# Kernel optimization log

Hardware: AMD Instinct MI355X
Metric: run time of the kernel (lower is better)

Reference implementation:

```python
import jax, jax.numpy as jnp
import numpy as np

N = 100000  # nodes


def setup_inputs() -> dict:
    key = jax.random.key(0)
    k0, k1, k2, k3 = jax.random.split(key, 4)
    IN, H, OUT = 256, 256, 128  # in_channels, 2*out_channels, out_channels
    E = 1600000
    x = jax.random.normal(k0, (N, IN), dtype=jnp.float32)
    edge_index = jax.random.randint(k1, (2, E), 0, N, dtype=jnp.int32)
    W1 = jax.random.normal(k2, (IN, H), dtype=jnp.float32) / np.sqrt(IN)
    b1 = jnp.zeros((H,), dtype=jnp.float32)
    W2 = jax.random.normal(k3, (H, OUT), dtype=jnp.float32) / np.sqrt(H)
    b2 = jnp.zeros((OUT,), dtype=jnp.float32)
    return {"x": x, "edge_index": edge_index, "W1": W1, "b1": b1, "W2": W2, "b2": b2}


def _gcn_layer(x, W, b, src, dst, norm):
    # PyG GCNConv: out[i] = sum_{(j->i)} norm_e * (x @ W)[j] + b, over A + I
    h = x @ W
    msg = h[src] * norm[:, None]          # [E+N, F] gathered edge messages
    out = jax.ops.segment_sum(msg, dst, num_segments=N)
    return out + b


def reference(x, edge_index, W1, b1, W2, b2):
    src, dst = edge_index[0], edge_index[1]
    loop = jnp.arange(N, dtype=src.dtype)
    src = jnp.concatenate([src, loop])    # add self-loops
    dst = jnp.concatenate([dst, loop])
    # symmetric normalization: deg computed on target (col) with unit weights
    deg = jax.ops.segment_sum(jnp.ones_like(dst, dtype=x.dtype), dst, num_segments=N)
    dinv = jnp.where(deg > 0, jax.lax.rsqrt(deg), 0.0)
    norm = dinv[src] * dinv[dst]
    h = jax.nn.relu(_gcn_layer(x, W1, b1, src, dst, norm))
    out = jax.nn.relu(_gcn_layer(h, W2, b2, src, dst, norm))
    return out
```

## Files before the change

kernel.cpp:

```cpp
#include <hip/hip_runtime.h>
#include <hip/hip_fp16.h>


typedef _Float16 f16x8 __attribute__((ext_vector_type(8)));
typedef float f32x4 __attribute__((ext_vector_type(4)));
typedef int i32x4 __attribute__((ext_vector_type(4)));
typedef float fv4 __attribute__((ext_vector_type(4)));

constexpr int CAP = 48;
constexpr int FILL_CHUNK = 2048;


__device__ inline void pack_w_body(const float* __restrict__ W, __half* __restrict__ Wp,
                                   int NC, int t) {
    const int NT = NC / 16;
    int lane = t & 63;
    int rest = t >> 6;
    int nt = rest % NT;
    int ks = rest / NT;
    int n = nt * 16 + (lane & 15);
    int k0 = ks * 32 + (lane >> 4) * 8;
    __half tmp[8];
#pragma unroll
    for (int j = 0; j < 8; ++j) tmp[j] = __float2half_rn(W[(size_t)(k0 + j) * NC + n]);
    ((uint4*)Wp)[t] = *(const uint4*)tmp;
}

__global__ __launch_bounds__(256) void prep_kernel(const int* __restrict__ src,
                                                   const int* __restrict__ dst, int E,
                                                   int* __restrict__ cntP, int chP,
                                                   int* __restrict__ colFixed,
                                                   const float* __restrict__ x,
                                                   __half* __restrict__ xh, int n8,
                                                   const float* __restrict__ W1,
                                                   __half* __restrict__ Wp1,
                                                   const float* __restrict__ W2,
                                                   __half* __restrict__ Wp2,
                                                   int nbFill, int nbPack) {
    const int b = blockIdx.x;
    const int tid = threadIdx.x;
    if (b < nbFill) {
        const int sel = b & 7;
        const int chunk = b >> 3;
        const int e0 = chunk * FILL_CHUNK + tid * 8;
        int* __restrict__ myCnt = cntP + sel * chP;
        if (e0 + 8 <= E) {
            i32x4 da = __builtin_nontemporal_load((const i32x4*)(dst + e0));
            i32x4 db = __builtin_nontemporal_load((const i32x4*)(dst + e0) + 1);
            i32x4 sa = __builtin_nontemporal_load((const i32x4*)(src + e0));
            i32x4 sb = __builtin_nontemporal_load((const i32x4*)(src + e0) + 1);
            int d[8] = {da[0], da[1], da[2], da[3], db[0], db[1], db[2], db[3]};
            int s[8] = {sa[0], sa[1], sa[2], sa[3], sb[0], sb[1], sb[2], sb[3]};
#pragma unroll
            for (int j = 0; j < 8; ++j) {
                if ((d[j] & 7) == sel) {
                    int slot = atomicAdd(&myCnt[d[j] >> 3], 1);
                    if (slot < CAP) colFixed[(size_t)d[j] * CAP + slot] = s[j];
                }
            }
        } else {
            for (int j = 0; j < 8; ++j) {
                int e = e0 + j;
                if (e < E) {
                    int dd = dst[e];
                    if ((dd & 7) == sel) {
                        int slot = atomicAdd(&myCnt[dd >> 3], 1);
                        if (slot < CAP) colFixed[(size_t)dd * CAP + slot] = src[e];
                    }
                }
            }
        }
    } else if (b < nbFill + nbPack) {
        int i = (b - nbFill) * 256 + tid;
        if (i < n8) {
            fv4 a = __builtin_nontemporal_load((const fv4*)x + (size_t)i * 2);
            fv4 bb = __builtin_nontemporal_load((const fv4*)x + (size_t)i * 2 + 1);
            __half2 h[4];
            h[0] = __floats2half2_rn(a[0], a[1]);
            h[1] = __floats2half2_rn(a[2], a[3]);
            h[2] = __floats2half2_rn(bb[0], bb[1]);
            h[3] = __floats2half2_rn(bb[2], bb[3]);
            ((uint4*)xh)[i] = *(const uint4*)h;
        }
    } else if (b < nbFill + nbPack + 32) {
        int t = (b - nbFill - nbPack) * 256 + tid;
        pack_w_body(W1, Wp1, 256, t);
    } else {
        int t = (b - nbFill - nbPack - 32) * 256 + tid;
        pack_w_body(W2, Wp2, 128, t);
    }
}

__global__ __launch_bounds__(256) void finish_deg(const int* __restrict__ cntP, int chP,
                                                  float* __restrict__ dinv,
                                                  int* __restrict__ degc, int N) {
    int i = blockIdx.x * 256 + threadIdx.x;
    if (i < N) {
        int c = cntP[(i & 7) * chP + (i >> 3)];
        dinv[i] = rsqrtf((float)(c + 1));
        degc[i] = (c < CAP) ? c : CAP;
    }
}

__global__ __launch_bounds__(256) void aggregate256_h(const __half* __restrict__ xh,
                                                      const float* __restrict__ dinv,
                                                      const int* __restrict__ degc,
                                                      const int* __restrict__ colFixed,
                                                      __half* __restrict__ out, int N) {
    const int lane = threadIdx.x & 63;
    const int i = blockIdx.x * 4 + (threadIdx.x >> 6);
    if (i >= N) return;
    const float di = dinv[i];
    const int deg = degc[i];
    const uint2* __restrict__ hv = (const uint2*)xh;
    uint2 raw = hv[(size_t)i * 64 + lane];
    float2 f0 = __half22float2(*(const __half2*)&raw.x);
    float2 f1 = __half22float2(*(const __half2*)&raw.y);
    float ax = di * f0.x, ay = di * f0.y, az = di * f1.x, aw = di * f1.y;
    const int* __restrict__ cl = colFixed + (size_t)i * CAP;
    int e = 0;
    for (; e + 8 <= deg; e += 8) {
        int s[8];
#pragma unroll
        for (int j = 0; j < 8; ++j) s[j] = cl[e + j];
        float w[8];
#pragma unroll
        for (int j = 0; j < 8; ++j) w[j] = dinv[s[j]];
        uint2 u[8];
#pragma unroll
        for (int j = 0; j < 8; ++j) u[j] = hv[(size_t)s[j] * 64 + lane];
#pragma unroll
        for (int j = 0; j < 8; ++j) {
            float2 g0 = __half22float2(*(const __half2*)&u[j].x);
            float2 g1 = __half22float2(*(const __half2*)&u[j].y);
            ax = fmaf(w[j], g0.x, ax);
            ay = fmaf(w[j], g0.y, ay);
            az = fmaf(w[j], g1.x, az);
            aw = fmaf(w[j], g1.y, aw);
        }
    }
    for (; e < deg; ++e) {
        int s = cl[e];
        float w = dinv[s];
        uint2 u = hv[(size_t)s * 64 + lane];
        float2 g0 = __half22float2(*(const __half2*)&u.x);
        float2 g1 = __half22float2(*(const __half2*)&u.y);
        ax = fmaf(w, g0.x, ax);
        ay = fmaf(w, g0.y, ay);
        az = fmaf(w, g1.x, az);
        aw = fmaf(w, g1.y, aw);
    }
    __half2 h0 = __floats2half2_rn(ax * di, ay * di);
    __half2 h1 = __floats2half2_rn(az * di, aw * di);
    uint2 o;
    o.x = *(const unsigned int*)&h0;
    o.y = *(const unsigned int*)&h1;
    ((uint2*)out)[(size_t)i * 64 + lane] = o;
}

__global__ __launch_bounds__(256) void gemm12_lds(const __half* __restrict__ A,
                                                  const __half* __restrict__ Wp1,
                                                  const float* __restrict__ bias1,
                                                  const __half* __restrict__ Wp2,
                                                  const float* __restrict__ dinv,
                                                  __half* __restrict__ out, int M) {
    constexpr int PITCH = 264;
    __shared__ _Float16 hs[4][16][PITCH];

    const int lane = threadIdx.x & 63;
    const int wave = threadIdx.x >> 6;
    const int kg = lane >> 4;
    const int r = lane & 15;
    const int row = blockIdx.x * 64 + wave * 16 + r;
    const int rowc = (row < M) ? row : (M - 1);

    f32x4 acc1[16];
#pragma unroll
    for (int nt = 0; nt < 16; ++nt) acc1[nt] = {0.f, 0.f, 0.f, 0.f};

    const f16x8* __restrict__ Ap = (const f16x8*)(A + (size_t)rowc * 256 + kg * 8);
    const f16x8* __restrict__ Wf1 = (const f16x8*)Wp1;
#pragma unroll
    for (int ks = 0; ks < 8; ++ks) {
        f16x8 xfrag = Ap[ks * 4];
        const f16x8* wrow = Wf1 + (size_t)(ks * 16) * 64 + lane;
#pragma unroll
        for (int nt = 0; nt < 16; ++nt) {
            f16x8 wfrag = wrow[nt * 64];
            acc1[nt] = __builtin_amdgcn_mfma_f32_16x16x32_f16(wfrag, xfrag, acc1[nt], 0, 0, 0);
        }
    }

#pragma unroll
    for (int nt = 0; nt < 16; ++nt) {
        float4 bb = *(const float4*)(bias1 + nt * 16 + kg * 4);
        f32x4 v = acc1[nt];
        v[0] = fmaxf(v[0] + bb.x, 0.f);
        v[1] = fmaxf(v[1] + bb.y, 0.f);
        v[2] = fmaxf(v[2] + bb.z, 0.f);
        v[3] = fmaxf(v[3] + bb.w, 0.f);
        __half2 h0 = __floats2half2_rn(v[0], v[1]);
        __half2 h1 = __floats2half2_rn(v[2], v[3]);
        uint2 o;
        o.x = *(const unsigned int*)&h0;
        o.y = *(const unsigned int*)&h1;
        *(uint2*)&hs[wave][r][nt * 16 + kg * 4] = o;
    }

    f32x4 acc2[8];
#pragma unroll
    for (int nt = 0; nt < 8; ++nt) acc2[nt] = {0.f, 0.f, 0.f, 0.f};

    const f16x8* __restrict__ Wf2 = (const f16x8*)Wp2;
#pragma unroll
    for (int ks = 0; ks < 8; ++ks) {
        f16x8 xfrag = *(const f16x8*)&hs[wave][r][ks * 32 + kg * 8];
        const f16x8* wrow = Wf2 + (size_t)(ks * 8) * 64 + lane;
#pragma unroll
        for (int nt = 0; nt < 8; ++nt) {
            f16x8 wfrag = wrow[nt * 64];
            acc2[nt] = __builtin_amdgcn_mfma_f32_16x16x32_f16(wfrag, xfrag, acc2[nt], 0, 0, 0);
        }
    }

    if (row < M) {
        float rs = dinv[row];
#pragma unroll
        for (int nt = 0; nt < 8; ++nt) {
            const int n0 = nt * 16 + kg * 4;
            f32x4 v = acc2[nt];
            __half2 h0 = __floats2half2_rn(v[0] * rs, v[1] * rs);
            __half2 h1 = __floats2half2_rn(v[2] * rs, v[3] * rs);
            uint2 o;
            o.x = *(const unsigned int*)&h0;
            o.y = *(const unsigned int*)&h1;
            *(uint2*)(out + (size_t)row * 128 + n0) = o;
        }
    }
}

__global__ __launch_bounds__(256) void aggregate128_h_bias_relu(const __half* __restrict__ h,
                                                                const float* __restrict__ dinv,
                                                                const int* __restrict__ degc,
                                                                const int* __restrict__ colFixed,
                                                                const float* __restrict__ bias,
                                                                float* __restrict__ out, int N) {
    const int lane = threadIdx.x & 63;
    const int i = blockIdx.x * 4 + (threadIdx.x >> 6);
    if (i >= N) return;
    const float di = dinv[i];
    const int deg = degc[i];
    const unsigned int* __restrict__ hv = (const unsigned int*)h;
    float2 v = __half22float2(*(const __half2*)&hv[(size_t)i * 64 + lane]);
    float ax = v.x, ay = v.y;
    const int* __restrict__ cl = colFixed + (size_t)i * CAP;
    int e = 0;
    for (; e + 8 <= deg; e += 8) {
        int s[8];
#pragma unroll
        for (int j = 0; j < 8; ++j) s[j] = cl[e + j];
        unsigned int u[8];
#pragma unroll
        for (int j = 0; j < 8; ++j) u[j] = hv[(size_t)s[j] * 64 + lane];
#pragma unroll
        for (int j = 0; j < 8; ++j) {
            float2 g = __half22float2(*(const __half2*)&u[j]);
            ax += g.x;
            ay += g.y;
        }
    }
    for (; e < deg; ++e) {
        float2 g = __half22float2(*(const __half2*)&hv[(size_t)cl[e] * 64 + lane]);
        ax += g.x;
        ay += g.y;
    }
    float2 bb = ((const float2*)bias)[lane];
    float2 r;
    r.x = fmaxf(fmaf(ax, di, bb.x), 0.f);
    r.y = fmaxf(fmaf(ay, di, bb.y), 0.f);
    ((float2*)out)[(size_t)i * 64 + lane] = r;
}

extern "C" void kernel_launch(void* const* d_in, const int* in_sizes, int n_in,
                              void* d_out, int out_size, void* d_ws, size_t ws_size,
                              hipStream_t stream) {
    const float* x  = (const float*)d_in[0];
    const int*   ei = (const int*)d_in[1];
    const float* W1 = (const float*)d_in[2];
    const float* b1 = (const float*)d_in[3];
    const float* W2 = (const float*)d_in[4];
    const float* b2 = (const float*)d_in[5];
    float* out = (float*)d_out;

    const int N = in_sizes[0] / 256;
    const int E = in_sizes[1] / 2;
    const int* src = ei;
    const int* dst = ei + E;

    char* ws = (char*)d_ws;
    size_t off = 0;
    auto alloc = [&](size_t bytes) -> char* {
        char* p = ws + off;
        off += (bytes + 255) & ~(size_t)255;
        return p;
    };
    const int chP = (N + 7) / 8;
    int*    cntP     = (int*)alloc((size_t)chP * 8 * 4);
    float*  dinv     = (float*)alloc((size_t)N * 4);
    int*    degc     = (int*)alloc((size_t)N * 4);
    int*    colFixed = (int*)alloc((size_t)N * CAP * 4);
    __half* Wp1      = (__half*)alloc((size_t)256 * 256 * 2);
    __half* Wp2      = (__half*)alloc((size_t)256 * 128 * 2);
    __half* bufA     = (__half*)alloc((size_t)N * 256 * 2);
    __half* bufB     = (__half*)alloc((size_t)N * 256 * 2);
    __half* xh    = bufA;
    __half* buf2h = bufA;
    __half* buf1h = bufB;

    hipMemsetAsync(cntP, 0, (size_t)chP * 8 * 4, stream);

    const int n8 = (N * 256) / 8;
    const int nbFill = 8 * ((E + FILL_CHUNK - 1) / FILL_CHUNK);
    const int nbPack = (n8 + 255) / 256;
    const int nbPrep = nbFill + nbPack + 32 + 16;
    prep_kernel<<<nbPrep, 256, 0, stream>>>(src, dst, E, cntP, chP, colFixed, x, xh, n8,
                                            W1, Wp1, W2, Wp2, nbFill, nbPack);

    finish_deg<<<(N + 255) / 256, 256, 0, stream>>>(cntP, chP, dinv, degc, N);

    const int AB = (N + 3) / 4;
    const int GB = (N + 63) / 64;

    aggregate256_h<<<AB, 256, 0, stream>>>(xh, dinv, degc, colFixed, buf1h, N);
    gemm12_lds<<<GB, 256, 0, stream>>>(buf1h, Wp1, b1, Wp2, dinv, buf2h, N);
    aggregate128_h_bias_relu<<<AB, 256, 0, stream>>>(buf2h, dinv, degc, colFixed, b2, out, N);
}
```

Measured before the change: 419.8 us.

## Slice feature matrix into 16-column panels for cache-local first-layer aggregation

Stores the fp16 input features in a sliced layout of 16 panels, each holding 16 columns for every node. The first aggregation kernel now launches one block set per panel, so each gather touches a 3.2 MB panel that can stay in L2/MALL instead of whole 512-byte rows. Within a wave, eight groups of lanes split the edge list and combine their sums with a shuffle reduction. The GEMM reads its A operand from the sliced layout. In exchange the kernel launches 16x more blocks, re-reads the column lists and dinv once per panel, and leaves lanes idle for low-degree nodes.

```diff
diff --git a/kernel.cpp b/kernel.cpp
--- a/kernel.cpp
+++ b/kernel.cpp
@@ -6,6 +6,7 @@
 typedef float f32x4 __attribute__((ext_vector_type(4)));
 typedef int i32x4 __attribute__((ext_vector_type(4)));
 typedef float fv4 __attribute__((ext_vector_type(4)));
+typedef unsigned int u32;
 
 constexpr int CAP = 48;
 constexpr int FILL_CHUNK = 2048;
@@ -31,7 +32,7 @@
                                                    int* __restrict__ cntP, int chP,
                                                    int* __restrict__ colFixed,
                                                    const float* __restrict__ x,
-                                                   __half* __restrict__ xh, int n8,
+                                                   __half* __restrict__ xs, int N,
                                                    const float* __restrict__ W1,
                                                    __half* __restrict__ Wp1,
                                                    const float* __restrict__ W2,
@@ -71,16 +72,22 @@
             }
         }
     } else if (b < nbFill + nbPack) {
-        int i = (b - nbFill) * 256 + tid;
-        if (i < n8) {
-            fv4 a = __builtin_nontemporal_load((const fv4*)x + (size_t)i * 2);
-            fv4 bb = __builtin_nontemporal_load((const fv4*)x + (size_t)i * 2 + 1);
-            __half2 h[4];
-            h[0] = __floats2half2_rn(a[0], a[1]);
-            h[1] = __floats2half2_rn(a[2], a[3]);
-            h[2] = __floats2half2_rn(bb[0], bb[1]);
-            h[3] = __floats2half2_rn(bb[2], bb[3]);
-            ((uint4*)xh)[i] = *(const uint4*)h;
+        const int bb_ = b - nbFill;
+        const int c16 = tid >> 4;
+        const int jj = tid & 15;
+        const int n = bb_ * 16 + jj;
+        if (n < N) {
+            const float* xp = x + (size_t)n * 256 + c16 * 16;
+            __half2 h[8];
+#pragma unroll
+            for (int q = 0; q < 4; ++q) {
+                fv4 a = __builtin_nontemporal_load((const fv4*)xp + q);
+                h[q * 2 + 0] = __floats2half2_rn(a[0], a[1]);
+                h[q * 2 + 1] = __floats2half2_rn(a[2], a[3]);
+            }
+            uint4* d32 = (uint4*)(xs + ((size_t)c16 * N + n) * 16);
+            d32[0] = *(const uint4*)&h[0];
+            d32[1] = *(const uint4*)&h[4];
         }
     } else if (b < nbFill + nbPack + 32) {
         int t = (b - nbFill - nbPack) * 256 + tid;
@@ -102,60 +109,54 @@
     }
 }
 
-__global__ __launch_bounds__(256) void aggregate256_h(const __half* __restrict__ xh,
-                                                      const float* __restrict__ dinv,
-                                                      const int* __restrict__ degc,
-                                                      const int* __restrict__ colFixed,
-                                                      __half* __restrict__ out, int N) {
+__global__ __launch_bounds__(256) void aggregate256_sliced(
+        const __half* __restrict__ xs,
+        const float* __restrict__ dinv,
+        const int* __restrict__ degc,
+        const int* __restrict__ colFixed,
+        __half* __restrict__ outS,
+        int N, int nchunk) {
+    const int b = blockIdx.x;
+    const int half = (b >= 8 * nchunk) ? 1 : 0;
+    const int sel = b & 7;
+    const int chunk = (b - half * 8 * nchunk) >> 3;
+    const int slice = half * 8 + sel;
     const int lane = threadIdx.x & 63;
-    const int i = blockIdx.x * 4 + (threadIdx.x >> 6);
+    const int wave = threadIdx.x >> 6;
+    const int g = lane >> 3;
+    const int c = lane & 7;
+    const int i = chunk * 4 + wave;
     if (i >= N) return;
     const float di = dinv[i];
     const int deg = degc[i];
-    const uint2* __restrict__ hv = (const uint2*)xh;
-    uint2 raw = hv[(size_t)i * 64 + lane];
-    float2 f0 = __half22float2(*(const __half2*)&raw.x);
-    float2 f1 = __half22float2(*(const __half2*)&raw.y);
-    float ax = di * f0.x, ay = di * f0.y, az = di * f1.x, aw = di * f1.y;
+    const u32* __restrict__ xs32 = (const u32*)xs;
+    const size_t sbase = (size_t)slice * N * 8;
+
+    float ax = 0.f, ay = 0.f;
+    if (g == 0) {
+        u32 u = xs32[sbase + (size_t)i * 8 + c];
+        float2 f = __half22float2(*(const __half2*)&u);
+        ax = di * f.x;
+        ay = di * f.y;
+    }
     const int* __restrict__ cl = colFixed + (size_t)i * CAP;
-    int e = 0;
-    for (; e + 8 <= deg; e += 8) {
-        int s[8];
-#pragma unroll
-        for (int j = 0; j < 8; ++j) s[j] = cl[e + j];
-        float w[8];
-#pragma unroll
-        for (int j = 0; j < 8; ++j) w[j] = dinv[s[j]];
-        uint2 u[8];
-#pragma unroll
-        for (int j = 0; j < 8; ++j) u[j] = hv[(size_t)s[j] * 64 + lane];
-#pragma unroll
-        for (int j = 0; j < 8; ++j) {
-            float2 g0 = __half22float2(*(const __half2*)&u[j].x);
-            float2 g1 = __half22float2(*(const __half2*)&u[j].y);
-            ax = fmaf(w[j], g0.x, ax);
-            ay = fmaf(w[j], g0.y, ay);
-            az = fmaf(w[j], g1.x, az);
-            aw = fmaf(w[j], g1.y, aw);
-        }
-    }
-    for (; e < deg; ++e) {
-        int s = cl[e];
+    for (int e = g; e < deg; e += 8) {
+        int s = __builtin_nontemporal_load(cl + e);
         float w = dinv[s];
-        uint2 u = hv[(size_t)s * 64 + lane];
-        float2 g0 = __half22float2(*(const __half2*)&u.x);
-        float2 g1 = __half22float2(*(const __half2*)&u.y);
-        ax = fmaf(w, g0.x, ax);
-        ay = fmaf(w, g0.y, ay);
-        az = fmaf(w, g1.x, az);
-        aw = fmaf(w, g1.y, aw);
-    }
-    __half2 h0 = __floats2half2_rn(ax * di, ay * di);
-    __half2 h1 = __floats2half2_rn(az * di, aw * di);
-    uint2 o;
-    o.x = *(const unsigned int*)&h0;
-    o.y = *(const unsigned int*)&h1;
-    ((uint2*)out)[(size_t)i * 64 + lane] = o;
+        u32 u = xs32[sbase + (size_t)s * 8 + c];
+        float2 f = __half22float2(*(const __half2*)&u);
+        ax = fmaf(w, f.x, ax);
+        ay = fmaf(w, f.y, ay);
+    }
+#pragma unroll
+    for (int off = 8; off < 64; off <<= 1) {
+        ax += __shfl_xor(ax, off, 64);
+        ay += __shfl_xor(ay, off, 64);
+    }
+    if (g == 0) {
+        __half2 h = __floats2half2_rn(ax * di, ay * di);
+        ((u32*)outS)[sbase + (size_t)i * 8 + c] = *(const u32*)&h;
+    }
 }
 
 __global__ __launch_bounds__(256) void gemm12_lds(const __half* __restrict__ A,
@@ -178,11 +179,12 @@
 #pragma unroll
     for (int nt = 0; nt < 16; ++nt) acc1[nt] = {0.f, 0.f, 0.f, 0.f};
 
-    const f16x8* __restrict__ Ap = (const f16x8*)(A + (size_t)rowc * 256 + kg * 8);
     const f16x8* __restrict__ Wf1 = (const f16x8*)Wp1;
+    const int off8 = (kg & 1) * 8;
 #pragma unroll
     for (int ks = 0; ks < 8; ++ks) {
-        f16x8 xfrag = Ap[ks * 4];
+        const int slice = 2 * ks + (kg >> 1);
+        f16x8 xfrag = *(const f16x8*)(A + ((size_t)slice * M + rowc) * 16 + off8);
         const f16x8* wrow = Wf1 + (size_t)(ks * 16) * 64 + lane;
 #pragma unroll
         for (int nt = 0; nt < 16; ++nt) {
@@ -202,8 +204,8 @@
         __half2 h0 = __floats2half2_rn(v[0], v[1]);
         __half2 h1 = __floats2half2_rn(v[2], v[3]);
         uint2 o;
-        o.x = *(const unsigned int*)&h0;
-        o.y = *(const unsigned int*)&h1;
+        o.x = *(const u32*)&h0;
+        o.y = *(const u32*)&h1;
         *(uint2*)&hs[wave][r][nt * 16 + kg * 4] = o;
     }
 
@@ -232,8 +234,8 @@
             __half2 h0 = __floats2half2_rn(v[0] * rs, v[1] * rs);
             __half2 h1 = __floats2half2_rn(v[2] * rs, v[3] * rs);
             uint2 o;
-            o.x = *(const unsigned int*)&h0;
-            o.y = *(const unsigned int*)&h1;
+            o.x = *(const u32*)&h0;
+            o.y = *(const u32*)&h1;
             *(uint2*)(out + (size_t)row * 128 + n0) = o;
         }
     }
@@ -250,7 +252,7 @@
     if (i >= N) return;
     const float di = dinv[i];
     const int deg = degc[i];
-    const unsigned int* __restrict__ hv = (const unsigned int*)h;
+    const u32* __restrict__ hv = (const u32*)h;
     float2 v = __half22float2(*(const __half2*)&hv[(size_t)i * 64 + lane]);
     float ax = v.x, ay = v.y;
     const int* __restrict__ cl = colFixed + (size_t)i * CAP;
@@ -259,7 +261,7 @@
         int s[8];
 #pragma unroll
         for (int j = 0; j < 8; ++j) s[j] = cl[e + j];
-        unsigned int u[8];
+        u32 u[8];
 #pragma unroll
         for (int j = 0; j < 8; ++j) u[j] = hv[(size_t)s[j] * 64 + lane];
 #pragma unroll
@@ -313,25 +315,27 @@
     __half* Wp2      = (__half*)alloc((size_t)256 * 128 * 2);
     __half* bufA     = (__half*)alloc((size_t)N * 256 * 2);
     __half* bufB     = (__half*)alloc((size_t)N * 256 * 2);
-    __half* xh    = bufA;
+    __half* xs    = bufA;
     __half* buf2h = bufA;
-    __half* buf1h = bufB;
+    __half* buf1s = bufB;
 
     hipMemsetAsync(cntP, 0, (size_t)chP * 8 * 4, stream);
 
-    const int n8 = (N * 256) / 8;
     const int nbFill = 8 * ((E + FILL_CHUNK - 1) / FILL_CHUNK);
-    const int nbPack = (n8 + 255) / 256;
+    const int nbPack = (N + 15) / 16;
     const int nbPrep = nbFill + nbPack + 32 + 16;
-    prep_kernel<<<nbPrep, 256, 0, stream>>>(src, dst, E, cntP, chP, colFixed, x, xh, n8,
+    prep_kernel<<<nbPrep, 256, 0, stream>>>(src, dst, E, cntP, chP, colFixed, x, xs, N,
                                             W1, Wp1, W2, Wp2, nbFill, nbPack);
 
     finish_deg<<<(N + 255) / 256, 256, 0, stream>>>(cntP, chP, dinv, degc, N);
 
+    const int nchunk = (N + 3) / 4;
+    aggregate256_sliced<<<16 * nchunk, 256, 0, stream>>>(xs, dinv, degc, colFixed,
+                                                         buf1s, N, nchunk);
+
+    const int GB = (N + 63) / 64;
+    gemm12_lds<<<GB, 256, 0, stream>>>(buf1s, Wp1, b1, Wp2, dinv, buf2h, N);
+
     const int AB = (N + 3) / 4;
-    const int GB = (N + 63) / 64;
-
-    aggregate256_h<<<AB, 256, 0, stream>>>(xh, dinv, degc, colFixed, buf1h, N);
-    gemm12_lds<<<GB, 256, 0, stream>>>(buf1h, Wp1, b1, Wp2, dinv, buf2h, N);
     aggregate128_h_bias_relu<<<AB, 256, 0, stream>>>(buf2h, dinv, degc, colFixed, b2, out, N);
 }
```

New measurement: 895.9 us. 2.13x slower.
